# Kernel optimization log

Hardware: AMD Instinct MI355X
Metric: run time of the kernel (lower is better)

Reference implementation:

```python
import jax, jax.numpy as jnp
import numpy as np

K_DIM = 1024
V_DIM = 1024
N_HEADS = 16
LN_EPS = 1e-5


def setup_inputs() -> dict:
    key = jax.random.key(0)
    ks = jax.random.split(key, 5)
    B, S = 16, 4096
    K = jax.random.normal(ks[0], (B, S, K_DIM), jnp.float32)
    V = jax.random.normal(ks[1], (B, S, V_DIM), jnp.float32)
    q = jax.random.normal(ks[2], (K_DIM,), jnp.float32)  # learned query
    w0_w = jax.random.normal(ks[3], (V_DIM, V_DIM), jnp.float32) / np.sqrt(V_DIM)
    w0_b = jnp.zeros((V_DIM,), jnp.float32)
    ln_g = jnp.ones((V_DIM,), jnp.float32)
    ln_b = jnp.zeros((V_DIM,), jnp.float32)
    return {"K": K, "V": V, "q": q, "w0_w": w0_w, "w0_b": w0_b, "ln_g": ln_g, "ln_b": ln_b}


def reference(K, V, q, w0_w, w0_b, ln_g, ln_b):
    B, S, C = K.shape
    H = N_HEADS
    d = C // H
    dv = V.shape[-1] // H
    # norm_query=True
    Q = q / jnp.linalg.norm(q)
    # expand to [B,1,C] then faithful contiguous view -> [B*H,1,d]
    Qh = jnp.broadcast_to(Q, (B, 1, C)).reshape(B * H, 1, d)
    # NOTE: the original uses a plain .view (row-major reshape), NOT a
    # transpose-based head split; we reproduce it exactly.
    Kh = K.reshape(B * H, S, d)
    Vh = V.reshape(B * H, S, dv)
    # torchtext ScaledDotProduct: softmax(Q K^T / sqrt(d)) V
    scale = 1.0 / jnp.sqrt(jnp.asarray(d, K.dtype))
    scores = jnp.einsum("bqd,bkd->bqk", Qh * scale, Kh)  # [B*H,1,S]
    attn = jax.nn.softmax(scores, axis=-1)
    A = jnp.einsum("bqk,bkd->bqd", attn, Vh)  # [B*H,1,dv]
    A = A.reshape(B, 1, H * dv)  # multihead_unshape
    # w0 linear
    A = A @ w0_w.T + w0_b
    # LayerNorm over last dim
    mu = jnp.mean(A, axis=-1, keepdims=True)
    var = jnp.var(A, axis=-1, keepdims=True)
    return ln_g * (A - mu) / jnp.sqrt(var + LN_EPS) + ln_b
```

## Files before the change

kernel.cpp:

```cpp
#include <hip/hip_runtime.h>

#define S_LEN 4096
#define D_HEAD 64
#define NH 16
#define C_DIM 1024
#define B_SZ 16
#define NG 256
#define NSPLIT 8
#define CHUNK (S_LEN / NSPLIT)
#define TPB 256
#define RG 16
#define ITERS (CHUNK / RG)

__global__ __launch_bounds__(256) void qnorm_kernel(
    const float* __restrict__ q, float* __restrict__ qs)
{
    const int tid = threadIdx.x;
    float v[4];
    float p = 0.f;
    #pragma unroll
    for (int i = 0; i < 4; i++) {
        v[i] = q[tid + i * 256];
        p += v[i] * v[i];
    }
    #pragma unroll
    for (int off = 32; off; off >>= 1) p += __shfl_xor(p, off);
    __shared__ float red[4];
    if ((tid & 63) == 0) red[tid >> 6] = p;
    __syncthreads();
    const float total = red[0] + red[1] + red[2] + red[3];
    const float s = rsqrtf(total) * 0.125f;
    #pragma unroll
    for (int i = 0; i < 4; i++) qs[tid + i * 256] = v[i] * s;
}

__global__ __launch_bounds__(TPB) void attn_partial(
    const float* __restrict__ K, const float* __restrict__ V,
    const float* __restrict__ qs, float* __restrict__ Apart,
    float* __restrict__ mArr, float* __restrict__ lArr)
{
    const int blk   = blockIdx.x;
    const int g     = blk >> 3;
    const int split = blk & 7;
    const int h     = g & (NH - 1);
    const int tid   = threadIdx.x;
    const int sub   = tid & 15;
    const int rg    = tid >> 4;

    __shared__ float sc[CHUNK];
    __shared__ __align__(16) float part[RG * D_HEAD];
    __shared__ float red[TPB / 64];

    const float4 qv = ((const float4*)(qs + h * D_HEAD))[sub];
    const float* __restrict__ Kg = K + ((size_t)g * S_LEN + (size_t)split * CHUNK) * D_HEAD;
    const float* __restrict__ Vg = V + ((size_t)g * S_LEN + (size_t)split * CHUNK) * D_HEAD;

    #pragma unroll 8
    for (int i = 0; i < ITERS; i++) {
        const int r = rg + i * RG;
        float4 kv = ((const float4*)(Kg + r * D_HEAD))[sub];
        float d = kv.x * qv.x + kv.y * qv.y + kv.z * qv.z + kv.w * qv.w;
        d += __shfl_xor(d, 1);
        d += __shfl_xor(d, 2);
        d += __shfl_xor(d, 4);
        d += __shfl_xor(d, 8);
        if (sub == 0) sc[r] = d;
    }
    __syncthreads();

    float m = fmaxf(sc[tid], sc[tid + 256]);
    #pragma unroll
    for (int off = 32; off; off >>= 1) m = fmaxf(m, __shfl_xor(m, off));
    if ((tid & 63) == 0) red[tid >> 6] = m;
    __syncthreads();
    m = fmaxf(fmaxf(red[0], red[1]), fmaxf(red[2], red[3]));
    __syncthreads();

    const float e0 = __expf(sc[tid] - m);
    const float e1 = __expf(sc[tid + 256] - m);
    sc[tid] = e0;
    sc[tid + 256] = e1;
    float sum = e0 + e1;
    #pragma unroll
    for (int off = 32; off; off >>= 1) sum += __shfl_xor(sum, off);
    if ((tid & 63) == 0) red[tid >> 6] = sum;
    __syncthreads();
    const float lsum = red[0] + red[1] + red[2] + red[3];

    float4 acc = make_float4(0.f, 0.f, 0.f, 0.f);
    #pragma unroll 8
    for (int i = 0; i < ITERS; i++) {
        const int r = rg + i * RG;
        float4 vv = ((const float4*)(Vg + r * D_HEAD))[sub];
        const float pr = sc[r];
        acc.x += pr * vv.x;
        acc.y += pr * vv.y;
        acc.z += pr * vv.z;
        acc.w += pr * vv.w;
    }
    ((float4*)part)[rg * 16 + sub] = acc;
    __syncthreads();
    if (tid < D_HEAD) {
        float s = 0.f;
        #pragma unroll
        for (int r2 = 0; r2 < RG; r2++) s += part[r2 * D_HEAD + tid];
        Apart[(size_t)blk * D_HEAD + tid] = s;
    }
    if (tid == 0) {
        mArr[blk] = m;
        lArr[blk] = lsum;
    }
}

__global__ __launch_bounds__(64) void attn_combine(
    const float* __restrict__ Apart, const float* __restrict__ mArr,
    const float* __restrict__ lArr, float* __restrict__ A)
{
    const int g = blockIdx.x;
    const int d = threadIdx.x;
    float mv[NSPLIT];
    float M = -3.4e38f;
    #pragma unroll
    for (int s = 0; s < NSPLIT; s++) {
        mv[s] = mArr[g * NSPLIT + s];
        M = fmaxf(M, mv[s]);
    }
    float denom = 0.f, acc = 0.f;
    #pragma unroll
    for (int s = 0; s < NSPLIT; s++) {
        const float f = __expf(mv[s] - M);
        denom += f * lArr[g * NSPLIT + s];
        acc   += f * Apart[(size_t)(g * NSPLIT + s) * D_HEAD + d];
    }
    A[g * D_HEAD + d] = acc / denom;
}

__global__ __launch_bounds__(256) void proj_kernel(
    const float* __restrict__ A, const float* __restrict__ W,
    const float* __restrict__ bias, float* __restrict__ Y)
{
    const int j = blockIdx.x;
    const int tid = threadIdx.x;
    const float* __restrict__ Wj = W + (size_t)j * C_DIM;

    float acc[B_SZ];
    #pragma unroll
    for (int b = 0; b < B_SZ; b++) acc[b] = 0.f;

    #pragma unroll
    for (int k = 0; k < 4; k++) {
        const int c = tid + k * 256;
        const float w = Wj[c];
        #pragma unroll
        for (int b = 0; b < B_SZ; b++) acc[b] += A[b * C_DIM + c] * w;
    }

    __shared__ float redw[B_SZ][4];
    #pragma unroll
    for (int b = 0; b < B_SZ; b++) {
        float v = acc[b];
        #pragma unroll
        for (int off = 32; off; off >>= 1) v += __shfl_xor(v, off);
        if ((tid & 63) == 0) redw[b][tid >> 6] = v;
    }
    __syncthreads();
    if (tid < B_SZ) {
        const float s = redw[tid][0] + redw[tid][1] + redw[tid][2] + redw[tid][3];
        Y[tid * C_DIM + j] = s + bias[j];
    }
}

__global__ __launch_bounds__(256) void ln_kernel(
    const float* __restrict__ Y, const float* __restrict__ gam,
    const float* __restrict__ bet, float* __restrict__ out)
{
    const int b = blockIdx.x;
    const int tid = threadIdx.x;
    const float* __restrict__ Yb = Y + b * C_DIM;

    float vals[4];
    float s = 0.f, s2 = 0.f;
    #pragma unroll
    for (int i = 0; i < 4; i++) {
        const float v = Yb[tid + i * 256];
        vals[i] = v;
        s += v;
        s2 += v * v;
    }
    #pragma unroll
    for (int off = 32; off; off >>= 1) {
        s  += __shfl_xor(s, off);
        s2 += __shfl_xor(s2, off);
    }
    __shared__ float rs[4], rs2[4];
    if ((tid & 63) == 0) { rs[tid >> 6] = s; rs2[tid >> 6] = s2; }
    __syncthreads();
    s  = rs[0] + rs[1] + rs[2] + rs[3];
    s2 = rs2[0] + rs2[1] + rs2[2] + rs2[3];
    const float mu  = s * (1.0f / C_DIM);
    const float var = s2 * (1.0f / C_DIM) - mu * mu;
    const float inv = rsqrtf(var + 1e-5f);
    #pragma unroll
    for (int i = 0; i < 4; i++) {
        const int j = tid + i * 256;
        out[b * C_DIM + j] = gam[j] * (vals[i] - mu) * inv + bet[j];
    }
}

extern "C" void kernel_launch(void* const* d_in, const int* in_sizes, int n_in,
                              void* d_out, int out_size, void* d_ws, size_t ws_size,
                              hipStream_t stream) {
    const float* K    = (const float*)d_in[0];
    const float* V    = (const float*)d_in[1];
    const float* q    = (const float*)d_in[2];
    const float* w0_w = (const float*)d_in[3];
    const float* w0_b = (const float*)d_in[4];
    const float* ln_g = (const float*)d_in[5];
    const float* ln_b = (const float*)d_in[6];

    float* qs    = (float*)d_ws;
    float* Apart = qs + C_DIM;
    float* mArr  = Apart + (size_t)NG * NSPLIT * D_HEAD;
    float* lArr  = mArr + NG * NSPLIT;
    float* A     = lArr + NG * NSPLIT;
    float* Y     = A + B_SZ * C_DIM;

    qnorm_kernel<<<1, 256, 0, stream>>>(q, qs);
    attn_partial<<<NG * NSPLIT, TPB, 0, stream>>>(K, V, qs, Apart, mArr, lArr);
    attn_combine<<<NG, 64, 0, stream>>>(Apart, mArr, lArr, A);
    proj_kernel<<<C_DIM, 256, 0, stream>>>(A, w0_w, w0_b, Y);
    ln_kernel<<<B_SZ, 256, 0, stream>>>(Y, ln_g, ln_b, (float*)d_out);
}
```

Baseline: 523.8 us.

## Fuse K and V passes with online softmax and nontemporal loads

Replaces the two-pass score/softmax/PV structure with a single streaming loop. Each 16-thread row group loads K and V together and keeps a running max, sum and accumulator (online softmax). The per-group partial states are merged in shared memory before being written out. This drops the score buffer, several block barriers and the second sweep, and uses nontemporal loads for the streamed data, at the cost of two exps per row per lane and a serial rescale dependency.

```diff
diff --git a/kernel.cpp b/kernel.cpp
--- a/kernel.cpp
+++ b/kernel.cpp
@@ -12,6 +12,8 @@
 #define RG 16
 #define ITERS (CHUNK / RG)
 
+typedef float f4 __attribute__((ext_vector_type(4)));
+
 __global__ __launch_bounds__(256) void qnorm_kernel(
     const float* __restrict__ q, float* __restrict__ qs)
 {
@@ -47,68 +49,55 @@
     const int sub   = tid & 15;
     const int rg    = tid >> 4;
 
-    __shared__ float sc[CHUNK];
     __shared__ __align__(16) float part[RG * D_HEAD];
-    __shared__ float red[TPB / 64];
-
-    const float4 qv = ((const float4*)(qs + h * D_HEAD))[sub];
-    const float* __restrict__ Kg = K + ((size_t)g * S_LEN + (size_t)split * CHUNK) * D_HEAD;
-    const float* __restrict__ Vg = V + ((size_t)g * S_LEN + (size_t)split * CHUNK) * D_HEAD;
-
-    #pragma unroll 8
+    __shared__ float mS[RG];
+    __shared__ float lS[RG];
+
+    const f4 qv = ((const f4*)(qs + h * D_HEAD))[sub];
+    const f4* __restrict__ Kg =
+        (const f4*)(K + ((size_t)g * S_LEN + (size_t)split * CHUNK) * D_HEAD);
+    const f4* __restrict__ Vg =
+        (const f4*)(V + ((size_t)g * S_LEN + (size_t)split * CHUNK) * D_HEAD);
+
+    float m = -3.4e38f;
+    float l = 0.f;
+    f4 acc = (f4){0.f, 0.f, 0.f, 0.f};
+
+    #pragma unroll 4
     for (int i = 0; i < ITERS; i++) {
         const int r = rg + i * RG;
-        float4 kv = ((const float4*)(Kg + r * D_HEAD))[sub];
+        const f4 kv = __builtin_nontemporal_load(Kg + r * (D_HEAD / 4) + sub);
+        const f4 vv = __builtin_nontemporal_load(Vg + r * (D_HEAD / 4) + sub);
         float d = kv.x * qv.x + kv.y * qv.y + kv.z * qv.z + kv.w * qv.w;
         d += __shfl_xor(d, 1);
         d += __shfl_xor(d, 2);
         d += __shfl_xor(d, 4);
         d += __shfl_xor(d, 8);
-        if (sub == 0) sc[r] = d;
-    }
-    __syncthreads();
-
-    float m = fmaxf(sc[tid], sc[tid + 256]);
-    #pragma unroll
-    for (int off = 32; off; off >>= 1) m = fmaxf(m, __shfl_xor(m, off));
-    if ((tid & 63) == 0) red[tid >> 6] = m;
-    __syncthreads();
-    m = fmaxf(fmaxf(red[0], red[1]), fmaxf(red[2], red[3]));
-    __syncthreads();
-
-    const float e0 = __expf(sc[tid] - m);
-    const float e1 = __expf(sc[tid + 256] - m);
-    sc[tid] = e0;
-    sc[tid + 256] = e1;
-    float sum = e0 + e1;
-    #pragma unroll
-    for (int off = 32; off; off >>= 1) sum += __shfl_xor(sum, off);
-    if ((tid & 63) == 0) red[tid >> 6] = sum;
-    __syncthreads();
-    const float lsum = red[0] + red[1] + red[2] + red[3];
-
-    float4 acc = make_float4(0.f, 0.f, 0.f, 0.f);
-    #pragma unroll 8
-    for (int i = 0; i < ITERS; i++) {
-        const int r = rg + i * RG;
-        float4 vv = ((const float4*)(Vg + r * D_HEAD))[sub];
-        const float pr = sc[r];
-        acc.x += pr * vv.x;
-        acc.y += pr * vv.y;
-        acc.z += pr * vv.z;
-        acc.w += pr * vv.w;
-    }
-    ((float4*)part)[rg * 16 + sub] = acc;
-    __syncthreads();
+        const float mnew = fmaxf(m, d);
+        const float fsc  = __expf(m - mnew);
+        const float w    = __expf(d - mnew);
+        l   = l * fsc + w;
+        acc = acc * fsc + w * vv;
+        m   = mnew;
+    }
+
+    ((f4*)part)[rg * 16 + sub] = acc;
+    if (sub == 0) { mS[rg] = m; lS[rg] = l; }
+    __syncthreads();
+
     if (tid < D_HEAD) {
-        float s = 0.f;
-        #pragma unroll
-        for (int r2 = 0; r2 < RG; r2++) s += part[r2 * D_HEAD + tid];
+        float M = mS[0];
+        #pragma unroll
+        for (int r2 = 1; r2 < RG; r2++) M = fmaxf(M, mS[r2]);
+        float s = 0.f, lt = 0.f;
+        #pragma unroll
+        for (int r2 = 0; r2 < RG; r2++) {
+            const float f = __expf(mS[r2] - M);
+            s  += f * part[r2 * D_HEAD + tid];
+            lt += f * lS[r2];
+        }
         Apart[(size_t)blk * D_HEAD + tid] = s;
-    }
-    if (tid == 0) {
-        mArr[blk] = m;
-        lArr[blk] = lsum;
+        if (tid == 0) { mArr[blk] = M; lArr[blk] = lt; }
     }
 }
 
```

After: 493.3 us. -5.8%, faster.
